# Kernel optimization log

Measured on AMD Instinct MI355X. Metric: run time of the kernel, lower is better.

Reference implementation:

```python
import jax, jax.numpy as jnp
import numpy as np

VOCAB = 50257
D = 1024
EDGES = [0, 20000, 40000, VOCAB]  # cluster boundaries
HSZ = [1024, 256, 64]             # D // 4**i per cluster


def setup_inputs() -> dict:
    key = jax.random.key(0)
    ks = jax.random.split(key, 8)
    emb_input = jax.random.randint(ks[0], (8, 2048), 0, VOCAB, dtype=jnp.int64)
    inp = {"emb_input": emb_input}
    for i in range(3):
        vsz = EDGES[i + 1] - EDGES[i]
        h = HSZ[i]
        inp[f"emb{i}"] = jax.random.normal(ks[1 + 2 * i], (vsz, h), dtype=jnp.float32) * 0.02
        # nn.Linear(h, D, bias=False) weight has shape [D, h]
        inp[f"w{i}"] = jax.random.normal(ks[2 + 2 * i], (D, h), dtype=jnp.float32) * 0.02
    return inp


def reference(emb_input, emb0, w0, emb1, w1, emb2, w2):
    B, S = emb_input.shape
    idx = emb_input.reshape(-1)  # [N]
    clusters = [(emb0, w0), (emb1, w1), (emb2, w2)]
    out = jnp.zeros((idx.shape[0], D), dtype=jnp.float32)
    for i, (emb, w) in enumerate(clusters):
        lo, hi = EDGES[i], EDGES[i + 1]
        mask = (idx >= lo) & (idx < hi)                       # [N]
        local = jnp.clip(idx - lo, 0, emb.shape[0] - 1)       # in-range gather ids
        h = emb[local]                                        # [N, hsz_i]
        proj = jnp.einsum('nh,dh->nd', h, w)                  # [N, D]
        out = out + jnp.where(mask[:, None], proj, 0.0)
    return out.reshape(B, S, D)
```

## Files before the change

kernel.cpp:

```cpp
#include <hip/hip_runtime.h>
#include <hip/hip_bf16.h>
#include <stdint.h>

#define DOUT 1024
#define NMAX 16384

#define BM 256
#define BN 128
#define LDSBUF 49152
#define BOFFS 32768

typedef __attribute__((ext_vector_type(8))) short short8;
typedef __attribute__((ext_vector_type(4))) float floatx4;

__device__ __forceinline__ unsigned short f2bf(float f) {
  union { float f; uint32_t u; } v;
  v.f = f;
  return (unsigned short)((v.u + 0x7FFFu + ((v.u >> 16) & 1u)) >> 16);
}

__device__ __forceinline__ ushort4 cvt4(float4 v) {
  __hip_bfloat162 p0 = __float22bfloat162_rn(make_float2(v.x, v.y));
  __hip_bfloat162 p1 = __float22bfloat162_rn(make_float2(v.z, v.w));
  union { __hip_bfloat162 h[2]; ushort4 s; } u;
  u.h[0] = p0; u.h[1] = p1;
  return u.s;
}

__global__ __launch_bounds__(256) void classify_cvt_kernel(
    const int* __restrict__ idx, int* __restrict__ cnt,
    int* __restrict__ bucket, int* __restrict__ blocal, int N,
    const float* __restrict__ w0, const float* __restrict__ w1,
    const float* __restrict__ w2, unsigned short* __restrict__ wb0,
    unsigned short* __restrict__ wb1, unsigned short* __restrict__ wb2) {
  if (blockIdx.x < 64) {
    int n = blockIdx.x * 256 + threadIdx.x;
    int lane = threadIdx.x & 63;
    int c = -1, v = 0;
    if (n < N) {
      v = idx[n];
      c = (v < 20000) ? 0 : ((v < 40000) ? 1 : 2);
    }
#pragma unroll
    for (int k = 0; k < 3; ++k) {
      unsigned long long m = __ballot(c == k);
      if (c == k) {
        int leader = __ffsll((unsigned long long)m) - 1;
        int base = 0;
        if (lane == leader) base = atomicAdd(&cnt[k], (int)__popcll(m));
        base = __shfl(base, leader);
        int rank = (int)__popcll(m & ((1ull << (unsigned)lane) - 1ull));
        int lo = (k == 0) ? 0 : (k == 1) ? 20000 : 40000;
        bucket[k * NMAX + base + rank] = n;
        blocal[k * NMAX + base + rank] = v - lo;
      }
    }
  } else {
    int i = (blockIdx.x - 64) * 256 + threadIdx.x;
    if (i >= 344064) return;
    const float4* src;
    ushort4* dst;
    if (i < 262144) {
      src = (const float4*)w0 + i;
      dst = (ushort4*)wb0 + i;
    } else if (i < 327680) {
      src = (const float4*)w1 + (i - 262144);
      dst = (ushort4*)wb1 + (i - 262144);
    } else {
      src = (const float4*)w2 + (i - 327680);
      dst = (ushort4*)wb2 + (i - 327680);
    }
    float4 v = *src;
    ushort4 o;
    o.x = f2bf(v.x); o.y = f2bf(v.y); o.z = f2bf(v.z); o.w = f2bf(v.w);
    *dst = o;
  }
}

__global__ __launch_bounds__(256) void gather_kernel(
    const float* __restrict__ emb0, const float* __restrict__ emb1,
    const float* __restrict__ emb2, const int* __restrict__ cnt,
    const int* __restrict__ blocal, unsigned short* __restrict__ Abf) {
  const int b = blockIdx.x;
  const int c0 = cnt[0], c1 = cnt[1], c2 = cnt[2];
  const float* emb;
  const int* bl;
  int H, count, baseRow, lg;
  size_t off;
  if (b < 4096) {
    emb = emb0; bl = blocal; H = 1024; count = c0; off = 0;
    baseRow = b * 4; lg = 6;
  } else if (b < 5120) {
    emb = emb1; bl = blocal + NMAX; H = 256; count = c1;
    off = (size_t)c0 * 1024; baseRow = (b - 4096) * 16; lg = 4;
  } else {
    emb = emb2; bl = blocal + 2 * NMAX; H = 64; count = c2;
    off = (size_t)c0 * 1024 + (size_t)c1 * 256; baseRow = (b - 5120) * 64; lg = 2;
  }
  const int tid = threadIdx.x;
  const int r = baseRow + (tid >> lg);
  if (r >= count) return;
  const int tpr = 1 << lg;
  const int e = (tid & (tpr - 1)) * 4;
  const int stride = tpr * 4;
  const float* src = emb + (size_t)bl[r] * H + e;
  unsigned short* d = Abf + off + (size_t)r * H + e;
#pragma unroll
  for (int j = 0; j < 4; ++j) {
    float4 v = *(const float4*)(src + j * stride);
    *(ushort4*)(d + j * stride) = cvt4(v);
  }
}

template <int H>
__device__ __forceinline__ void gemm_body(
    const unsigned short* __restrict__ A, const unsigned short* __restrict__ B,
    int count, const int* __restrict__ bucket, float* __restrict__ out,
    char* lds, int* rowTok) {
  const int orig = blockIdx.y * gridDim.x + blockIdx.x;
  const int by = (orig & 7) + 8 * (orig >> 6);
  const int bx = (orig >> 3) & 7;

  const int m0 = by * BM;
  if (m0 >= count) return;
  const int n0 = bx * BN;
  constexpr int NT = H / 64;

  const int tid = threadIdx.x;
  const int wave = tid >> 6;
  const int lane = tid & 63;
  const int quad = lane >> 4;
  const int l16 = lane & 15;
  const int wm = wave & 3;
  const int wn = wave >> 2;

  if (tid < BM) {
    int m = m0 + tid;
    rowTok[tid] = (m < count) ? bucket[m] : -1;
  }

  const int dl = wave * 1024 + lane * 16;
  const int lswz = dl ^ (((dl >> 7) & 3) << 4);
  const int rW = lswz >> 6;
  const int ckW = (lswz >> 4) & 3;
  const char* Abyte = (const char*)A;
  const char* Bbyte = (const char*)B;
  const size_t aOff0 = ((size_t)(m0 + rW) * H) * 2 + ckW * 16;
  const size_t aOff1 = ((size_t)(m0 + 128 + rW) * H) * 2 + ckW * 16;
  const size_t bOff = ((size_t)(n0 + rW) * H) * 2 + ckW * 16;

  auto stage = [&](int kt, char* buf) {
    const int kb = kt * 128;
#pragma unroll
    for (int s = 0; s < 2; ++s) {
      __builtin_amdgcn_global_load_lds(
          (const __attribute__((address_space(1))) void*)(Abyte + aOff0 + kb + s * 64),
          (__attribute__((address_space(3))) void*)(buf + s * 16384 + wave * 1024),
          16, 0, 0);
      __builtin_amdgcn_global_load_lds(
          (const __attribute__((address_space(1))) void*)(Abyte + aOff1 + kb + s * 64),
          (__attribute__((address_space(3))) void*)(buf + s * 16384 + 8192 + wave * 1024),
          16, 0, 0);
      __builtin_amdgcn_global_load_lds(
          (const __attribute__((address_space(1))) void*)(Bbyte + bOff + kb + s * 64),
          (__attribute__((address_space(3))) void*)(buf + BOFFS + s * 8192 + wave * 1024),
          16, 0, 0);
    }
  };

  int offA[2][4], offB[2][4];
#pragma unroll
  for (int s = 0; s < 2; ++s) {
#pragma unroll
    for (int i = 0; i < 4; ++i) {
      int ba = (wm * 64 + i * 16 + l16) * 64 + quad * 16;
      offA[s][i] = s * 16384 + (ba ^ (((ba >> 7) & 3) << 4));
      int bb = (wn * 64 + i * 16 + l16) * 64 + quad * 16;
      offB[s][i] = BOFFS + s * 8192 + (bb ^ (((bb >> 7) & 3) << 4));
    }
  }

  if (NT >= 1) stage(0, lds);
  if (NT >= 2) stage(1, lds + LDSBUF);
  if (NT >= 3) stage(2, lds + 2 * LDSBUF);

  floatx4 acc[4][4];
#pragma unroll
  for (int i = 0; i < 4; ++i)
#pragma unroll
    for (int j = 0; j < 4; ++j) acc[i][j] = (floatx4){0.f, 0.f, 0.f, 0.f};

#pragma unroll
  for (int kt = 0; kt < NT; ++kt) {
    const int rem = NT - 1 - kt;
    if (rem >= 2)
      asm volatile("s_waitcnt vmcnt(12)" ::: "memory");
    else if (rem == 1)
      asm volatile("s_waitcnt vmcnt(6)" ::: "memory");
    else
      asm volatile("s_waitcnt vmcnt(0)" ::: "memory");
    asm volatile("s_barrier" ::: "memory");

    const char* buf = lds + (kt % 3) * LDSBUF;
    short8 a[2][4], b[2][4];
#pragma unroll
    for (int s = 0; s < 2; ++s)
#pragma unroll
      for (int i = 0; i < 4; ++i) {
        a[s][i] = *(const short8*)(buf + offA[s][i]);
        b[s][i] = *(const short8*)(buf + offB[s][i]);
      }
    __builtin_amdgcn_s_setprio(1);
#pragma unroll
    for (int s = 0; s < 2; ++s)
#pragma unroll
      for (int i = 0; i < 4; ++i)
#pragma unroll
        for (int j = 0; j < 4; ++j)
          acc[i][j] = __builtin_amdgcn_mfma_f32_16x16x32_bf16(
              a[s][i], b[s][j], acc[i][j], 0, 0, 0);
    __builtin_amdgcn_s_setprio(0);
    asm volatile("s_barrier" ::: "memory");
    if (kt + 3 < NT) stage(kt + 3, lds + (kt % 3) * LDSBUF);
  }

  const int colBase = n0 + wn * 64 + l16;
#pragma unroll
  for (int mi = 0; mi < 4; ++mi) {
#pragma unroll
    for (int r = 0; r < 4; ++r) {
      int tok = rowTok[wm * 64 + mi * 16 + quad * 4 + r];
      if (tok >= 0) {
        float* o = out + (size_t)tok * DOUT + colBase;
#pragma unroll
        for (int ni = 0; ni < 4; ++ni) o[ni * 16] = acc[mi][ni][r];
      }
    }
  }
}

__global__ __launch_bounds__(512, 2) void gemm_pipe(
    const unsigned short* __restrict__ Abf,
    const unsigned short* __restrict__ wb0,
    const unsigned short* __restrict__ wb1,
    const unsigned short* __restrict__ wb2, const int* __restrict__ cnt,
    const int* __restrict__ bucket, float* __restrict__ out) {
  __shared__ __align__(16) char lds[3 * LDSBUF + BM * 4];
  int* rowTok = (int*)(lds + 3 * LDSBUF);

  const int z = blockIdx.z;
  const int c0 = cnt[0];
  const int c1 = cnt[1];
  if (z == 0)
    gemm_body<1024>(Abf, wb0, c0, bucket, out, lds, rowTok);
  else if (z == 1)
    gemm_body<256>(Abf + (size_t)c0 * 1024, wb1, c1, bucket + NMAX, out, lds,
                   rowTok);
  else
    gemm_body<64>(Abf + (size_t)c0 * 1024 + (size_t)c1 * 256, wb2, cnt[2],
                  bucket + 2 * NMAX, out, lds, rowTok);
}

extern "C" void kernel_launch(void* const* d_in, const int* in_sizes, int n_in,
                              void* d_out, int out_size, void* d_ws, size_t ws_size,
                              hipStream_t stream) {
  const int* idx = (const int*)d_in[0];
  const float* emb0 = (const float*)d_in[1];
  const float* w0 = (const float*)d_in[2];
  const float* emb1 = (const float*)d_in[3];
  const float* w1 = (const float*)d_in[4];
  const float* emb2 = (const float*)d_in[5];
  const float* w2 = (const float*)d_in[6];
  float* out = (float*)d_out;
  const int N = in_sizes[0];

  char* ws = (char*)d_ws;
  int* cnt = (int*)ws;
  int* bucket = (int*)(ws + 1024);
  int* blocal = bucket + 3 * NMAX;
  size_t off = 1024 + (size_t)6 * NMAX * 4;
  off = (off + 255) & ~(size_t)255;
  unsigned short* wb0 = (unsigned short*)(ws + off); off += (size_t)DOUT * 1024 * 2;
  unsigned short* wb1 = (unsigned short*)(ws + off); off += (size_t)DOUT * 256 * 2;
  unsigned short* wb2 = (unsigned short*)(ws + off); off += (size_t)DOUT * 64 * 2;
  off = (off + 255) & ~(size_t)255;
  unsigned short* Abf = (unsigned short*)(ws + off);
  off += (size_t)(NMAX + 256) * 1024 * 2;

  hipMemsetAsync(cnt, 0, 16 * sizeof(int), stream);

  classify_cvt_kernel<<<64 + 1344, 256, 0, stream>>>(
      idx, cnt, bucket, blocal, N, w0, w1, w2, wb0, wb1, wb2);

  gather_kernel<<<5376, 256, 0, stream>>>(emb0, emb1, emb2, cnt, blocal, Abf);

  dim3 grid(DOUT / BN, NMAX / BM, 3);
  gemm_pipe<<<grid, 512, 0, stream>>>(Abf, wb0, wb1, wb2, cnt, bucket, out);
}
```

Measured before the change: 202.2 us.

## Replace 3D gemm grid with persistent kernel using atomic tile counter

Swaps the fixed 3D grid, where many blocks exit early because cluster counts are data-dependent, for a persistent kernel of 256 blocks. Each block pulls tiles from a global atomic counter spanning all three clusters in order, largest H first. This is meant to remove idle launched blocks and balance the uneven per-cluster work. It drops the swizzled block ordering (by/bx now come straight from the tile index), which may hurt L2 reuse. It also adds two barriers and an atomic per tile, and launch_bounds no longer requests 2 blocks per CU.

```diff
diff --git a/kernel.cpp b/kernel.cpp
--- a/kernel.cpp
+++ b/kernel.cpp
@@ -113,18 +113,13 @@
 }
 
 template <int H>
-__device__ __forceinline__ void gemm_body(
+__device__ __forceinline__ void tile_compute(
     const unsigned short* __restrict__ A, const unsigned short* __restrict__ B,
     int count, const int* __restrict__ bucket, float* __restrict__ out,
-    char* lds, int* rowTok) {
-  const int orig = blockIdx.y * gridDim.x + blockIdx.x;
-  const int by = (orig & 7) + 8 * (orig >> 6);
-  const int bx = (orig >> 3) & 7;
-
+    char* lds, int* rowTok, int by, int bx) {
+  constexpr int NT = H / 64;
   const int m0 = by * BM;
-  if (m0 >= count) return;
   const int n0 = bx * BN;
-  constexpr int NT = H / 64;
 
   const int tid = threadIdx.x;
   const int wave = tid >> 6;
@@ -239,26 +234,44 @@
   }
 }
 
-__global__ __launch_bounds__(512, 2) void gemm_pipe(
+__global__ __launch_bounds__(512) void gemm_persist(
     const unsigned short* __restrict__ Abf,
     const unsigned short* __restrict__ wb0,
     const unsigned short* __restrict__ wb1,
     const unsigned short* __restrict__ wb2, const int* __restrict__ cnt,
-    const int* __restrict__ bucket, float* __restrict__ out) {
-  __shared__ __align__(16) char lds[3 * LDSBUF + BM * 4];
+    const int* __restrict__ bucket, float* __restrict__ out,
+    int* __restrict__ tileCtr) {
+  __shared__ __align__(16) char lds[3 * LDSBUF + BM * 4 + 16];
   int* rowTok = (int*)(lds + 3 * LDSBUF);
-
-  const int z = blockIdx.z;
-  const int c0 = cnt[0];
-  const int c1 = cnt[1];
-  if (z == 0)
-    gemm_body<1024>(Abf, wb0, c0, bucket, out, lds, rowTok);
-  else if (z == 1)
-    gemm_body<256>(Abf + (size_t)c0 * 1024, wb1, c1, bucket + NMAX, out, lds,
-                   rowTok);
-  else
-    gemm_body<64>(Abf + (size_t)c0 * 1024 + (size_t)c1 * 256, wb2, cnt[2],
-                  bucket + 2 * NMAX, out, lds, rowTok);
+  int* curTile = (int*)(lds + 3 * LDSBUF + BM * 4);
+
+  const int c0 = cnt[0], c1 = cnt[1], c2 = cnt[2];
+  const int nt0 = (c0 + BM - 1) / BM;
+  const int nt1 = (c1 + BM - 1) / BM;
+  const int nt2 = (c2 + BM - 1) / BM;
+  const int T0 = nt0 * 8, T1 = nt1 * 8, T2 = nt2 * 8;
+  const int total = T0 + T1 + T2;
+  const size_t o1 = (size_t)c0 * 1024;
+  const size_t o2 = o1 + (size_t)c1 * 256;
+
+  for (;;) {
+    __syncthreads();
+    if (threadIdx.x == 0) *curTile = atomicAdd(tileCtr, 1);
+    __syncthreads();
+    const int t = *curTile;
+    if (t >= total) return;
+    if (t < T0) {
+      tile_compute<1024>(Abf, wb0, c0, bucket, out, lds, rowTok, t >> 3, t & 7);
+    } else if (t < T0 + T1) {
+      const int u = t - T0;
+      tile_compute<256>(Abf + o1, wb1, c1, bucket + NMAX, out, lds, rowTok,
+                        u >> 3, u & 7);
+    } else {
+      const int u = t - T0 - T1;
+      tile_compute<64>(Abf + o2, wb2, c2, bucket + 2 * NMAX, out, lds, rowTok,
+                       u >> 3, u & 7);
+    }
+  }
 }
 
 extern "C" void kernel_launch(void* const* d_in, const int* in_sizes, int n_in,
@@ -294,6 +307,6 @@
 
   gather_kernel<<<5376, 256, 0, stream>>>(emb0, emb1, emb2, cnt, blocal, Abf);
 
-  dim3 grid(DOUT / BN, NMAX / BM, 3);
-  gemm_pipe<<<grid, 512, 0, stream>>>(Abf, wb0, wb1, wb2, cnt, bucket, out);
-}
+  gemm_persist<<<256, 512, 0, stream>>>(Abf, wb0, wb1, wb2, cnt, bucket, out,
+                                        cnt + 8);
+}
```

Result: no change. 198.5 us (-1.8%).
